# Optimization experiments

Measured on AMD Instinct MI355X. Metric: run time of the kernel, lower is better.

The kernel has to match this reference:

```python
import jax, jax.numpy as jnp
import numpy as np
import math

B, M, C = 4, 2048, 1024
H = 8
DQK = C // 4 // H   # 32
DV = C // H         # 128
LEAKY_SLOPE = 0.2


def setup_inputs() -> dict:
    key = jax.random.key(0)
    ks = jax.random.split(key, 9)
    s = 1.0 / math.sqrt(C)
    return {
        "x": jax.random.normal(ks[0], (B, M, C), jnp.float32),
        "y": jax.random.normal(ks[1], (B, M, C), jnp.float32),
        "Wq": jax.random.normal(ks[2], (C, C // 4), jnp.float32) * s,
        "bq": jax.random.normal(ks[3], (C // 4,), jnp.float32) * s,
        "Wk": jax.random.normal(ks[4], (C, C // 4), jnp.float32) * s,
        "bk": jax.random.normal(ks[5], (C // 4,), jnp.float32) * s,
        "Wv": jax.random.normal(ks[6], (C, C), jnp.float32) * s,
        "bv": jax.random.normal(ks[7], (C,), jnp.float32) * s,
        "gamma": jax.random.normal(ks[8], (1,), jnp.float32) * 0.1,
    }


def reference(x, y, Wq, bq, Wk, bk, Wv, bv, gamma):
    b, m, c = x.shape
    m2 = y.shape[1]
    # projections; split heads
    f = (x @ Wq + bq).reshape(b, m, H, DQK)    # queries
    g = (y @ Wk + bk).reshape(b, m2, H, DQK)   # keys
    h = (y @ Wv + bv).reshape(b, m2, H, DV)    # values
    scores = jnp.einsum('bmhd,bnhd->bhmn', f, g) / math.sqrt(DQK)
    scores = jnp.where(scores >= 0, scores, LEAKY_SLOPE * scores)  # leaky_relu(0.2)
    beta = jax.nn.softmax(scores, axis=-1)
    o = jnp.einsum('bhmn,bnhd->bmhd', beta, h)  # [B, M, H, DV]
    return gamma[0] * o.reshape(b, m, c) + x
```

## Files before the change

kernel.cpp:

```cpp
#include <hip/hip_runtime.h>
#include <cstdint>
#include <cstddef>

typedef unsigned short u16;
typedef unsigned int u32;
typedef __attribute__((ext_vector_type(8))) short bf16x8;
typedef __attribute__((ext_vector_type(4))) float f32x4;
typedef __attribute__((ext_vector_type(16))) float f32x16;

__device__ __forceinline__ u16 f2bf(float f) {
  union { float f; unsigned int u; } v; v.f = f;
  unsigned int r = v.u + 0x7fffu + ((v.u >> 16) & 1u);
  return (u16)(r >> 16);
}

__device__ __forceinline__ u32 pack_bf_trunc(float hi, float lo) {
#if __has_builtin(__builtin_amdgcn_perm)
  return __builtin_amdgcn_perm(__float_as_uint(hi), __float_as_uint(lo), 0x07060302u);
#else
  return (__float_as_uint(hi) & 0xffff0000u) | (__float_as_uint(lo) >> 16);
#endif
}

__device__ __forceinline__ void glds16(const void* g, void* l) {
  __builtin_amdgcn_global_load_lds(
      (const __attribute__((address_space(1))) unsigned int*)g,
      (__attribute__((address_space(3))) unsigned int*)l, 16, 0, 0);
}

__device__ __forceinline__ f32x4 fzero4() { f32x4 z = {0.f, 0.f, 0.f, 0.f}; return z; }
__device__ __forceinline__ f32x16 fzero16() {
  f32x16 z;
  #pragma unroll
  for (int i = 0; i < 16; ++i) z[i] = 0.f;
  return z;
}

__global__ void prep_kernel(const float* __restrict__ x, u16* __restrict__ xb,
                            const float* __restrict__ y, u16* __restrict__ yb,
                            const float* __restrict__ Wq, const float* __restrict__ Wk,
                            const float* __restrict__ Wv, u16* __restrict__ wt) {
  __shared__ float tile[32][33];
  int bx = blockIdx.x;
  if (bx < 16384) {
    int i = bx * 256 + threadIdx.x;
    const float* src; u16* dst;
    if (i < 2097152) { src = x; dst = xb; }
    else             { src = y; dst = yb; i -= 2097152; }
    float4 v = ((const float4*)src)[i];
    ushort4 o = make_ushort4(f2bf(v.x), f2bf(v.y), f2bf(v.z), f2bf(v.w));
    ((ushort4*)dst)[i] = o;
    return;
  }
  int t = bx - 16384;
  const float* in; u16* out; int N, tn;
  if (t < 256)      { in = Wq; out = wt;              N = 256;  tn = t; }
  else if (t < 512) { in = Wk; out = wt + 256 * 1024; N = 256;  tn = t - 256; }
  else              { in = Wv; out = wt + 512 * 1024; N = 1024; tn = t - 512; }
  int ntiles = N >> 5;
  int n0 = (tn % ntiles) * 32, k0 = (tn / ntiles) * 32;
  int tx = threadIdx.x & 31, ty = threadIdx.x >> 5;
  #pragma unroll
  for (int j = ty; j < 32; j += 8) tile[j][tx] = in[(size_t)(k0 + j) * N + n0 + tx];
  __syncthreads();
  #pragma unroll
  for (int j = ty; j < 32; j += 8) out[(size_t)(n0 + j) * 1024 + k0 + tx] = f2bf(tile[tx][j]);
}

__global__ __launch_bounds__(256, 3)
void gemm_all_kernel(const u16* __restrict__ xb, const u16* __restrict__ yb,
                     const u16* __restrict__ wt,
                     const float* __restrict__ bq, const float* __restrict__ bk,
                     const float* __restrict__ bv,
                     u16* __restrict__ fb, u16* __restrict__ gb, u16* __restrict__ ht) {
  __shared__ __align__(16) u16 ls[17408];
  u16* lA = ls;
  u16* lB = ls + 8192;
  const int tid = threadIdx.x, lane = tid & 63;
  const int quad = lane >> 4, l16 = lane & 15;
  const int wave = tid >> 6;
  const int row0 = blockIdx.y * 128, col0 = blockIdx.x * 128;
  const int wm = (wave >> 1) * 64, wn = (wave & 1) * 64;
  const u16* A = (col0 < 256) ? xb : yb;

  f32x4 acc[4][4];
  #pragma unroll
  for (int i = 0; i < 4; i++)
    #pragma unroll
    for (int j = 0; j < 4; j++) acc[i][j] = fzero4();

  for (int k0 = 0; k0 < 1024; k0 += 64) {
    __syncthreads();
    #pragma unroll
    for (int i = 0; i < 4; i++) {
      int c = i * 256 + tid;
      glds16(A + (size_t)(row0 + (c & 127)) * 1024 + k0 + (c >> 7) * 8, lA + c * 8);
    }
    #pragma unroll
    for (int i = 0; i < 4; i++) {
      int c = i * 256 + tid;
      glds16(wt + (size_t)(col0 + (c & 127)) * 1024 + k0 + (c >> 7) * 8, lB + c * 8);
    }
    __syncthreads();
    #pragma unroll
    for (int kk = 0; kk < 2; kk++) {
      bf16x8 af[4], bfr[4];
      #pragma unroll
      for (int mi = 0; mi < 4; mi++)
        af[mi] = *(const bf16x8*)(lA + ((kk * 4 + quad) * 128 + wm + mi * 16 + l16) * 8);
      #pragma unroll
      for (int ni = 0; ni < 4; ni++)
        bfr[ni] = *(const bf16x8*)(lB + ((kk * 4 + quad) * 128 + wn + ni * 16 + l16) * 8);
      #pragma unroll
      for (int mi = 0; mi < 4; mi++)
        #pragma unroll
        for (int ni = 0; ni < 4; ni++)
          acc[mi][ni] = __builtin_amdgcn_mfma_f32_16x16x32_bf16(af[mi], bfr[ni], acc[mi][ni], 0, 0, 0);
    }
  }

  if (col0 < 512) {
    #pragma unroll
    for (int mi = 0; mi < 4; mi++)
      #pragma unroll
      for (int ni = 0; ni < 4; ni++) {
        int col = col0 + wn + ni * 16 + l16;
        float bvv = (col < 256) ? bq[col] : bk[col - 256];
        #pragma unroll
        for (int r = 0; r < 4; r++) {
          int row = row0 + wm + mi * 16 + quad * 4 + r;
          float v = acc[mi][ni][r] + bvv;
          int bb = row >> 11, ml = row & 2047;
          if (col < 256) {
            int h = col >> 5, kk2 = col & 31;
            fb[(((size_t)(bb * 8 + h)) << 16) + ml * 32 + kk2] = f2bf(v);
          } else {
            int c2 = col - 256, h = c2 >> 5, kk2 = c2 & 31;
            gb[((((size_t)(bb * 8 + h)) * 16 + (ml >> 7)) << 12)
               + (kk2 >> 3) * 1024 + (ml & 127) * 8 + (kk2 & 7)] = f2bf(v);
          }
        }
      }
  } else {
    const int headblk = (col0 - 512) >> 7;
    const int bb = row0 >> 11, mloc0 = row0 & 2047;
    __syncthreads();
    #pragma unroll
    for (int mi = 0; mi < 4; mi++)
      #pragma unroll
      for (int ni = 0; ni < 4; ni++) {
        int col = wn + ni * 16 + l16;
        int rowl = wm + mi * 16 + quad * 4;
        float bvv = bv[(col0 - 512) + col];
        float v0 = acc[mi][ni][0] + bvv, v1 = acc[mi][ni][1] + bvv;
        float v2 = acc[mi][ni][2] + bvv, v3 = acc[mi][ni][3] + bvv;
        *(uint2*)(ls + col * 136 + rowl) =
            make_uint2(pack_bf_trunc(v1, v0), pack_bf_trunc(v3, v2));
      }
    __syncthreads();
    u16* tb = ht + ((((size_t)(bb * 8 + headblk)) * 16 + (mloc0 >> 7)) << 14);
    #pragma unroll
    for (int i = 0; i < 8; ++i) {
      int chunk = i * 256 + tid;
      *(uint4*)(tb + chunk * 8) = *(const uint4*)(ls + (chunk & 127) * 136 + (chunk >> 7) * 8);
    }
  }
}

__global__ __launch_bounds__(256, 2)
void attn_kernel(const u16* __restrict__ fb, const u16* __restrict__ gb,
                 const u16* __restrict__ ht, const float* __restrict__ x,
                 const float* __restrict__ gamma, float* __restrict__ out) {
  __shared__ __align__(16) u16 lK[2][4096];
  __shared__ __align__(16) u16 lV[2][16384];
  const int tid = threadIdx.x;
  const int lane = tid & 63, wave = tid >> 6;
  const int hd = lane >> 5, l31 = lane & 31;

  int lin = blockIdx.x + 16 * blockIdx.y + 128 * blockIdx.z;
  const int head = lin & 7;
  const int mblk = (lin >> 3) & 15;
  const int b = lin >> 7;
  const int m0 = mblk * 128;
  const int bh = b * 8 + head;

  const float sscale = 0.17677669529663687f * 1.4426950408889634f;

  const int qrow = m0 + wave * 32 + l31;
  union { bf16x8 v; u16 s[8]; } q0, q1;
  {
    const u16* qp = fb + (((size_t)bh * 2048 + qrow) << 5);
    q0.v = *(const bf16x8*)(qp + hd * 8);
    q1.v = *(const bf16x8*)(qp + 16 + hd * 8);
    #pragma unroll
    for (int j = 0; j < 8; ++j) {
      q0.s[j] = f2bf(__uint_as_float((u32)q0.s[j] << 16) * sscale);
      q1.s[j] = f2bf(__uint_as_float((u32)q1.s[j] << 16) * sscale);
    }
  }

  f32x16 oacc[4];
  #pragma unroll
  for (int i = 0; i < 4; ++i) oacc[i] = fzero16();
  float lsum = 0.f;

  const u16* kbase = gb + ((size_t)bh << 16);
  const u16* vbase = ht + ((size_t)bh << 18);

  auto stage = [&](int bufsel, int nt) {
    const u16* ks_ = kbase + ((size_t)nt << 12);
    const u16* vs_ = vbase + ((size_t)nt << 14);
    #pragma unroll
    for (int i = 0; i < 2; ++i) glds16(ks_ + (i * 256 + tid) * 8, &lK[bufsel][(i * 256 + tid) * 8]);
    #pragma unroll
    for (int i = 0; i < 8; ++i) glds16(vs_ + (i * 256 + tid) * 8, &lV[bufsel][(i * 256 + tid) * 8]);
  };

  stage(0, 0);
  __syncthreads();

  int cur = 0;
  for (int it = 0; it < 16; ++it) {
    if (it < 15) stage(cur ^ 1, it + 1);
    const u16* Kc = lK[cur];
    const u16* Vc = lV[cur];

    u32 pk[4][8];
    #pragma unroll
    for (int nt4 = 0; nt4 < 4; ++nt4) {
      bf16x8 k0 = *(const bf16x8*)(Kc + hd * 1024 + (nt4 * 32 + l31) * 8);
      bf16x8 k1 = *(const bf16x8*)(Kc + (2 + hd) * 1024 + (nt4 * 32 + l31) * 8);
      f32x16 s = __builtin_amdgcn_mfma_f32_32x32x16_bf16(k0, q0.v, fzero16(), 0, 0, 0);
      s = __builtin_amdgcn_mfma_f32_32x32x16_bf16(k1, q1.v, s, 0, 0, 0);
      float p[16];
      #pragma unroll
      for (int r = 0; r < 16; ++r) {
        float sv = s[r];
        float lv = fmaxf(sv, 0.2f * sv);
        p[r] = __builtin_amdgcn_exp2f(lv);
        lsum += p[r];
      }
      #pragma unroll
      for (int s2 = 0; s2 < 4; ++s2) {
        pk[nt4][s2 * 2 + 0] = pack_bf_trunc(p[s2 * 4 + 1], p[s2 * 4 + 0]);
        pk[nt4][s2 * 2 + 1] = pack_bf_trunc(p[s2 * 4 + 3], p[s2 * 4 + 2]);
      }
    }

    #pragma unroll
    for (int kt = 0; kt < 8; ++kt) {
      const int nt4 = kt >> 1, a = kt & 1;
      u32 plo0 = pk[nt4][a * 4 + 0], plo1 = pk[nt4][a * 4 + 1];
      u32 phi0 = pk[nt4][a * 4 + 2], phi1 = pk[nt4][a * 4 + 3];
      u32 send0 = hd ? plo0 : phi0;
      u32 send1 = hd ? plo1 : phi1;
      u32 r0 = __shfl_xor(send0, 32, 64);
      u32 r1 = __shfl_xor(send1, 32, 64);
      u32 own0 = hd ? phi0 : plo0;
      u32 own1 = hd ? phi1 : plo1;
      union { u32 w[4]; bf16x8 v; } pf;
      pf.w[0] = hd ? r0 : own0;
      pf.w[1] = hd ? r1 : own1;
      pf.w[2] = hd ? own0 : r0;
      pf.w[3] = hd ? own1 : r1;
      #pragma unroll
      for (int dvt = 0; dvt < 4; ++dvt) {
        bf16x8 vf = *(const bf16x8*)(Vc + (kt * 2 + hd) * 1024 + (dvt * 32 + l31) * 8);
        oacc[dvt] = __builtin_amdgcn_mfma_f32_32x32x16_bf16(pf.v, vf, oacc[dvt], 0, 0, 0);
      }
    }
    __syncthreads();
    cur ^= 1;
  }

  float ltot = lsum + __shfl_xor(lsum, 32, 64);
  float inv = 1.0f / ltot;
  const float gam = gamma[0];
  const size_t rowbase = ((size_t)(b * 2048 + m0 + wave * 32)) * 1024 + head * 128 + l31;
  #pragma unroll
  for (int reg = 0; reg < 16; ++reg) {
    const int m32 = (reg & 3) + 8 * (reg >> 2) + 4 * hd;
    float iv = __shfl(inv, m32, 64);
    #pragma unroll
    for (int dvt = 0; dvt < 4; ++dvt) {
      size_t idx = rowbase + (size_t)m32 * 1024 + dvt * 32;
      out[idx] = gam * (oacc[dvt][reg] * iv) + x[idx];
    }
  }
}

extern "C" void kernel_launch(void* const* d_in, const int* in_sizes, int n_in,
                              void* d_out, int out_size, void* d_ws, size_t ws_size,
                              hipStream_t stream) {
  const float* x     = (const float*)d_in[0];
  const float* y     = (const float*)d_in[1];
  const float* Wq    = (const float*)d_in[2];
  const float* bq    = (const float*)d_in[3];
  const float* Wk    = (const float*)d_in[4];
  const float* bk    = (const float*)d_in[5];
  const float* Wv    = (const float*)d_in[6];
  const float* bv    = (const float*)d_in[7];
  const float* gamma = (const float*)d_in[8];
  float* out = (float*)d_out;

  char* ws = (char*)d_ws;
  u16* xb = (u16*)(ws);
  u16* yb = (u16*)(ws + 16777216);
  u16* wt = (u16*)(ws + 33554432);
  u16* fb = (u16*)(ws + 36700160);
  u16* gb = (u16*)(ws + 40894464);
  u16* ht = (u16*)(ws + 45088768);

  prep_kernel<<<16384 + 1536, 256, 0, stream>>>(x, xb, y, yb, Wq, Wk, Wv, wt);
  gemm_all_kernel<<<dim3(12, 64), 256, 0, stream>>>(xb, yb, wt, bq, bk, bv, fb, gb, ht);
  attn_kernel<<<dim3(16, 8, 4), 256, 0, stream>>>(fb, gb, ht, x, gamma, out);
}
```

Measured before the change: 245.3 us.

## Unroll double-buffer loop, use permlane32 swap, and raise MFMA priority

Replaces the two cross-half shuffles plus selects with v_permlane32_swap_b32 to exchange P fragments between wave halves. The double-buffered K/V loop is manually unrolled by two so LDS buffer addresses are compile-time constants and the cur toggle disappears. MFMA sections are wrapped in s_setprio to favour matrix issue over other waves. The goal is to cut shuffle/ALU overhead and address arithmetic, at the cost of larger code and reliance on gfx950-specific inline asm.

```diff
diff --git a/kernel.cpp b/kernel.cpp
--- a/kernel.cpp
+++ b/kernel.cpp
@@ -216,22 +216,16 @@
     for (int i = 0; i < 8; ++i) glds16(vs_ + (i * 256 + tid) * 8, &lV[bufsel][(i * 256 + tid) * 8]);
   };
 
-  stage(0, 0);
-  __syncthreads();
-
-  int cur = 0;
-  for (int it = 0; it < 16; ++it) {
-    if (it < 15) stage(cur ^ 1, it + 1);
-    const u16* Kc = lK[cur];
-    const u16* Vc = lV[cur];
-
+  auto compute = [&](const u16* Kc, const u16* Vc) {
     u32 pk[4][8];
     #pragma unroll
     for (int nt4 = 0; nt4 < 4; ++nt4) {
       bf16x8 k0 = *(const bf16x8*)(Kc + hd * 1024 + (nt4 * 32 + l31) * 8);
       bf16x8 k1 = *(const bf16x8*)(Kc + (2 + hd) * 1024 + (nt4 * 32 + l31) * 8);
+      __builtin_amdgcn_s_setprio(1);
       f32x16 s = __builtin_amdgcn_mfma_f32_32x32x16_bf16(k0, q0.v, fzero16(), 0, 0, 0);
       s = __builtin_amdgcn_mfma_f32_32x32x16_bf16(k1, q1.v, s, 0, 0, 0);
+      __builtin_amdgcn_s_setprio(0);
       float p[16];
       #pragma unroll
       for (int r = 0; r < 16; ++r) {
@@ -250,27 +244,33 @@
     #pragma unroll
     for (int kt = 0; kt < 8; ++kt) {
       const int nt4 = kt >> 1, a = kt & 1;
-      u32 plo0 = pk[nt4][a * 4 + 0], plo1 = pk[nt4][a * 4 + 1];
-      u32 phi0 = pk[nt4][a * 4 + 2], phi1 = pk[nt4][a * 4 + 3];
-      u32 send0 = hd ? plo0 : phi0;
-      u32 send1 = hd ? plo1 : phi1;
-      u32 r0 = __shfl_xor(send0, 32, 64);
-      u32 r1 = __shfl_xor(send1, 32, 64);
-      u32 own0 = hd ? phi0 : plo0;
-      u32 own1 = hd ? phi1 : plo1;
+      u32 w0 = pk[nt4][a * 4 + 0], w1 = pk[nt4][a * 4 + 1];
+      u32 w2 = pk[nt4][a * 4 + 2], w3 = pk[nt4][a * 4 + 3];
+      asm("v_permlane32_swap_b32 %0, %1" : "+v"(w0), "+v"(w2));
+      asm("v_permlane32_swap_b32 %0, %1" : "+v"(w1), "+v"(w3));
       union { u32 w[4]; bf16x8 v; } pf;
-      pf.w[0] = hd ? r0 : own0;
-      pf.w[1] = hd ? r1 : own1;
-      pf.w[2] = hd ? own0 : r0;
-      pf.w[3] = hd ? own1 : r1;
+      pf.w[0] = w0; pf.w[1] = w1; pf.w[2] = w2; pf.w[3] = w3;
+      __builtin_amdgcn_s_setprio(1);
       #pragma unroll
       for (int dvt = 0; dvt < 4; ++dvt) {
         bf16x8 vf = *(const bf16x8*)(Vc + (kt * 2 + hd) * 1024 + (dvt * 32 + l31) * 8);
         oacc[dvt] = __builtin_amdgcn_mfma_f32_32x32x16_bf16(pf.v, vf, oacc[dvt], 0, 0, 0);
       }
-    }
-    __syncthreads();
-    cur ^= 1;
+      __builtin_amdgcn_s_setprio(0);
+    }
+  };
+
+  stage(0, 0);
+  __syncthreads();
+
+  #pragma unroll 1
+  for (int it = 0; it < 16; it += 2) {
+    stage(1, it + 1);
+    compute(&lK[0][0], &lV[0][0]);
+    __syncthreads();
+    if (it + 2 < 16) stage(0, it + 2);
+    compute(&lK[1][0], &lV[1][0]);
+    __syncthreads();
   }
 
   float ltot = lsum + __shfl_xor(lsum, 32, 64);
```

Result: no change. 241.7 us (-1.5%).
